# Optimization experiments

Measured on AMD Instinct MI355X. Metric: run time of the kernel, lower is better.

The kernel has to match this reference:

```python
import jax, jax.numpy as jnp
import numpy as np

# ---- static config (matches PFNet init) ----
B, N, F = 8, 5000, 15          # batch, num_max_elems, raw features
NUM_CLS_IN = 12                # elem_labels
NUM_CLS_OUT = 8                # class_labels
NUM_MOM = 3
H = 256                        # hidden_dim_id = hidden_dim_reg = distance_dim
BIN_SIZE = 500
N_BINS = N // BIN_SIZE         # 10
MAX_NUM_BINS = 200
K_NN = 16                      # num_neighbors
DIST_MULT = 0.1
ENC_DIM = NUM_CLS_IN + (F - 1)  # 26


def _dense_init(key, shape, scale=0.05):
    return scale * jax.random.normal(key, shape, dtype=jnp.float32)


def setup_inputs() -> dict:
    key = jax.random.key(0)
    ks = jax.random.split(key, 32)
    # X: col0 = integer element type id, rest = continuous features
    ids = jax.random.randint(ks[0], (B, N, 1), 0, NUM_CLS_IN).astype(jnp.float32)
    props = jax.random.normal(ks[1], (B, N, F - 1), dtype=jnp.float32)
    X = jnp.concatenate([ids, props], axis=-1)
    inp = {"X": X}
    # distance-embedding FFN (point_wise_feed_forward_network(distance_dim, dff))
    inp["ffn1_w"] = _dense_init(ks[2], (ENC_DIM, H)); inp["ffn1_b"] = jnp.zeros((H,), jnp.float32)
    inp["ffn2_w"] = _dense_init(ks[3], (H, H));       inp["ffn2_b"] = jnp.zeros((H,), jnp.float32)
    # LSH codebook rotations (non-trainable)
    inp["R"] = _dense_init(ks[4], (H, MAX_NUM_BINS // 2), scale=1.0)
    # id branch: encoder -> GHConv -> decoder -> logits
    inp["enc_id_w"] = _dense_init(ks[5], (ENC_DIM, H)); inp["enc_id_b"] = jnp.zeros((H,), jnp.float32)
    inp["wt_id"] = _dense_init(ks[6], (H, H)); inp["bt_id"] = _dense_init(ks[7], (H,))
    inp["wh_id"] = _dense_init(ks[8], (H, H)); inp["theta_id"] = _dense_init(ks[9], (H, H))
    inp["dec_id_w"] = _dense_init(ks[10], (H, H)); inp["dec_id_b"] = jnp.zeros((H,), jnp.float32)
    inp["out_id_w"] = _dense_init(ks[11], (H, NUM_CLS_OUT)); inp["out_id_b"] = jnp.zeros((NUM_CLS_OUT,), jnp.float32)
    # reg branch: takes concat(encoded, id_logits)
    inp["enc_reg_w"] = _dense_init(ks[12], (ENC_DIM + NUM_CLS_OUT, H)); inp["enc_reg_b"] = jnp.zeros((H,), jnp.float32)
    inp["wt_reg"] = _dense_init(ks[13], (H, H)); inp["bt_reg"] = _dense_init(ks[14], (H,))
    inp["wh_reg"] = _dense_init(ks[15], (H, H)); inp["theta_reg"] = _dense_init(ks[16], (H, H))
    inp["dec_reg_w"] = _dense_init(ks[17], (H, H)); inp["dec_reg_b"] = jnp.zeros((H,), jnp.float32)
    inp["out_reg_w"] = _dense_init(ks[18], (H, NUM_MOM)); inp["out_reg_b"] = jnp.zeros((NUM_MOM,), jnp.float32)
    return inp


def _build_knn_graph(points, R):
    """LSH-binned approximate kNN for one event. points: [N, H].
    Returns edge list (src, dst, vals), each [N_BINS*BIN_SIZE*K_NN]."""
    mul = points @ R[:, : N_BINS // 2]                 # [N, nbins/2]
    cmul = jnp.concatenate([mul, -mul], axis=-1)       # [N, nbins]
    bin_idx = jnp.argmax(cmul, axis=-1)
    bins_split = jnp.argsort(bin_idx).reshape(N_BINS, BIN_SIZE)   # [nb, bs]
    parts = points[bins_split]                         # [nb, bs, H]
    # pairwise distance inside each bin
    sq = jnp.sum(parts * parts, axis=-1)               # [nb, bs]
    d2 = sq[:, :, None] - 2.0 * jnp.einsum('bnd,bmd->bnm', parts, parts) + sq[:, None, :]
    dm = jnp.exp(-DIST_MULT * jnp.sqrt(jnp.maximum(d2, 1e-6)))    # [nb, bs, bs]
    vals, idx = jax.lax.top_k(dm, K_NN)                # [nb, bs, k] local indices
    dst = bins_split[jnp.arange(N_BINS)[:, None, None], idx]      # global dst
    src = jnp.broadcast_to(bins_split[:, :, None], idx.shape)     # global src
    return src.reshape(-1).astype(jnp.int32), dst.reshape(-1).astype(jnp.int32), vals.reshape(-1)


def _ghconv(x, src, dst, vals, W_t, b_t, W_h, theta):
    """GHConv for one event. x: [N, H]; edge list from _build_knn_graph.
    Duplicate edges sum, matching tf.sparse.add semantics."""
    deg = jax.ops.segment_sum(jnp.abs(vals), src, num_segments=N)          # row sums
    norm = jnp.power(deg + 1e-6, -0.5)[:, None]                            # [N, 1]
    f_hom = (x @ theta) * norm                                             # [N, H]
    msg = vals[:, None] * f_hom[dst]                                       # [E, H]
    f_hom = jax.ops.segment_sum(msg, src, num_segments=N) * norm
    f_het = x @ W_h
    gate = jax.nn.sigmoid(x @ W_t + b_t)
    return jax.nn.selu(gate * f_hom + (1.0 - gate) * f_het)


def reference(X, ffn1_w, ffn1_b, ffn2_w, ffn2_b, R,
              enc_id_w, enc_id_b, wt_id, bt_id, wh_id, theta_id,
              dec_id_w, dec_id_b, out_id_w, out_id_b,
              enc_reg_w, enc_reg_b, wt_reg, bt_reg, wh_reg, theta_reg,
              dec_reg_w, dec_reg_b, out_reg_w, out_reg_b):
    # InputEncoding: one-hot id + continuous props
    Xid = jax.nn.one_hot(jax.lax.stop_gradient(X[:, :, 0]).astype(jnp.int32), NUM_CLS_IN, dtype=jnp.float32)
    enc = jnp.concatenate([Xid, X[:, :, 1:]], axis=-1)                     # [B, N, 26]
    # distance embedding FFN (elu hidden)
    x_dist = jax.nn.elu(enc @ ffn1_w + ffn1_b) @ ffn2_w + ffn2_b           # [B, N, H]
    # LSH-binned approximate kNN graph per event
    src, dst, vals = jax.vmap(_build_knn_graph, in_axes=(0, None))(x_dist, R)
    # --- id branch ---
    h = jax.nn.selu(enc @ enc_id_w + enc_id_b)
    h = jax.vmap(_ghconv, in_axes=(0, 0, 0, 0, None, None, None, None))(
        h, src, dst, vals, wt_id, bt_id, wh_id, theta_id)
    h = jax.nn.selu(h @ dec_id_w + dec_id_b)
    out_id_logits = h @ out_id_w + out_id_b                                # [B, N, 8]
    xr = jnp.concatenate([enc, out_id_logits], axis=-1)                    # [B, N, 34]
    g = jax.nn.selu(xr @ enc_reg_w + enc_reg_b)
    g = jax.vmap(_ghconv, in_axes=(0, 0, 0, 0, None, None, None, None))(
        g, src, dst, vals, wt_reg, bt_reg, wh_reg, theta_reg)
    g = jax.nn.selu(g @ dec_reg_w + dec_reg_b)
    pred_momentum = g @ out_reg_w + out_reg_b                              # [B, N, 3]
    return out_id_logits, pred_momentum
```

## Files before the change

kernel.cpp:

```cpp
#include <hip/hip_runtime.h>
#include <math.h>

#define B_    8
#define N_    5000
#define F_    15
#define NCIN  12
#define NCOUT 8
#define NMOM  3
#define H_    256
#define BINSZ 500
#define NBINS 10
#define KNN   16
#define ENCD  26
#define XRD   34
#define M_TOT (B_*N_)

typedef unsigned short u16;
typedef _Float16 half8 __attribute__((ext_vector_type(8)));
typedef float f32x4_ __attribute__((ext_vector_type(4)));

__device__ __forceinline__ float elu_f(float x){ return x > 0.f ? x : expm1f(x); }
__device__ __forceinline__ float selu_f(float x){
    const float scale = 1.0507009873554804934193349852946f;
    const float alpha = 1.6732632423543772848170429916717f;
// ... 231 lines not shown
    const u16* Brow = Wt + (size_t)(n0 + mloc)*K;
    f32x4_ z = {0.f, 0.f, 0.f, 0.f};
    f32x4_ acc[4][4];
    #pragma unroll
    for (int i = 0; i < 4; ++i)
        #pragma unroll
        for (int j = 0; j < 4; ++j) acc[i][j] = z;
    const int fr = lane & 15, fks = lane >> 4;
    int nc = K >> 5;
    uint4 sa0, sa1, sb0, sb1;

    sa0 = *(const uint4*)(Arow + ksl*8);
    sa1 = *(const uint4*)(Arow + 16 + ksl*8);
    sb0 = *(const uint4*)(Brow + ksl*8);
    sb1 = *(const uint4*)(Brow + 16 + ksl*8);
    *(uint4*)ALS_(0,ksl,  mloc) = sa0;
    *(uint4*)ALS_(0,ksl+2,mloc) = sa1;
    *(uint4*)BLS_(0,ksl,  mloc) = sb0;
    *(uint4*)BLS_(0,ksl+2,mloc) = sb1;
    __syncthreads();

    for (int c = 0; c < nc; ++c){
        if (c + 1 < nc){
            int k0 = (c+1)*32;
            sa0 = *(const uint4*)(Arow + k0 + ksl*8);
            sa1 = *(const uint4*)(Arow + k0 + 16 + ksl*8);
            sb0 = *(const uint4*)(Brow + k0 + ksl*8);
            sb1 = *(const uint4*)(Brow + k0 + 16 + ksl*8);
        }
        int cb = c & 1;
        half8 af[4], bf[4];
        #pragma unroll
        for (int mi = 0; mi < 4; ++mi)
            af[mi] = *reinterpret_cast<const half8*>(ALS_(cb, fks, wr + mi*16 + fr));
        #pragma unroll
        for (int ni = 0; ni < 4; ++ni)
            bf[ni] = *reinterpret_cast<const half8*>(BLS_(cb, fks, wc + ni*16 + fr));
        #pragma unroll
        for (int mi = 0; mi < 4; ++mi)
            #pragma unroll
            for (int ni = 0; ni < 4; ++ni)
                acc[mi][ni] = __builtin_amdgcn_mfma_f32_16x16x32_f16(af[mi], bf[ni], acc[mi][ni], 0, 0, 0);
        if (c + 1 < nc){
            __syncthreads();
            int nb2 = (c+1) & 1;
            *(uint4*)ALS_(nb2,ksl,  mloc) = sa0;
            *(uint4*)ALS_(nb2,ksl+2,mloc) = sa1;
            *(uint4*)BLS_(nb2,ksl,  mloc) = sb0;
            *(uint4*)BLS_(nb2,ksl+2,mloc) = sb1;
            __syncthreads();
        }
    }
    if (Cb){
        __syncthreads();
        #pragma unroll
        for (int ni = 0; ni < 4; ++ni){
            int lc = wc + ni*16 + fr;
            float bv = bias ? bias[n0 + lc] : 0.f;
            #pragma unroll
            for (int mi = 0; mi < 4; ++mi)
                #pragma unroll
                for (int r = 0; r < 4; ++r){
                    int lrow = wr + mi*16 + fks*4 + r;
                    float v = acc[mi][ni][r] + bv;
                    if (ACT == 2) v = selu_f(v);
                    else if (ACT == 3) v = sigmoid_f(v);
                    smem[lrow*128 + lc] = f2h(v);
                }
        }
        __syncthreads();
        int colb = (lane & 15)*8;
        #pragma unroll
        for (int it = 0; it < 8; ++it){
            int lrow = w*32 + it*4 + (lane >> 4);
            int grow = m0 + lrow;
            if (grow < M)
                *(uint4*)&Cb[(size_t)grow*Nw + n0 + colb] = *(uint4*)&smem[lrow*128 + colb];
        }
    } else {
        #pragma unroll
        for (int ni = 0; ni < 4; ++ni){
            int col = n0 + wc + ni*16 + fr;
            float bv = bias ? bias[col] : 0.f;
            #pragma unroll
            for (int mi = 0; mi < 4; ++mi)
                #pragma unroll
                for (int r = 0; r < 4; ++r){
                    int row = m0 + wr + mi*16 + fks*4 + r;
                    if (row < M){
                        float v = acc[mi][ni][r] + bv;
                        if (ACT == 2) v = selu_f(v);
                        else if (ACT == 3) v = sigmoid_f(v);
                        Cf[(size_t)row*Nw + col] = v;
                    }
                }
        }
    }
    #undef ALS_
    #undef BLS_
}

__global__ __launch_bounds__(256) void k_gemm_f16x3(const u16* __restrict__ A,
        const u16* __restrict__ Wtcat, const float* __restrict__ bt,
        u16* __restrict__ G, u16* __restrict__ Hh, u16* __restrict__ Hm, int M){
    const int K = H_;
    __shared__ u16 smem[16384];
    #define ALS_(cb,ks,m) (smem +        ((cb)*4096 + (ks)*1024 + (m)*8))
    #define BLS_(cb,ks,m) (smem + 8192 + ((cb)*4096 + (ks)*1024 + (m)*8))
    int tid = threadIdx.x;
    int lane = tid & 63, w = tid >> 6;
    int wr = (w >> 1)*64, wc = (w & 1)*64;
    int lin = blockIdx.x;
    int xcd = lin & 7, jj = lin >> 3;
    int wk = (xcd < 6 ? xcd*235 : 6*235 + (xcd-6)*234) + jj;
    int m0 = (wk/6)*128;
    int yy = wk % 6;
    int seg = yy >> 1;
    u16* Cb = seg == 0 ? G : (seg == 1 ? Hh : Hm);
    int c0 = (yy & 1)*128;
    int n0 = yy*128;
    int mloc = tid & 127;
    int ksl  = tid >> 7;
    int gmA = m0 + mloc; if (gmA >= M) gmA = M - 1;
    const u16* Arow = A     + (size_t)gmA*K;
    const u16* Brow = Wtcat + (size_t)(n0 + mloc)*K;
    f32x4_ z = {0.f, 0.f, 0.f, 0.f};
    f32x4_ acc[4][4];
    #pragma unroll
    for (int i = 0; i < 4; ++i)
        #pragma unroll
        for (int j = 0; j < 4; ++j) acc[i][j] = z;
    const int fr = lane & 15, fks = lane >> 4;
    const int nc = K >> 5;
    uint4 sa0, sa1, sb0, sb1;
    sa0 = *(const uint4*)(Arow + ksl*8);
    sa1 = *(const uint4*)(Arow + 16 + ksl*8);
    sb0 = *(const uint4*)(Brow + ksl*8);
    sb1 = *(const uint4*)(Brow + 16 + ksl*8);
    *(uint4*)ALS_(0,ksl,  mloc) = sa0;
    *(uint4*)ALS_(0,ksl+2,mloc) = sa1;
    *(uint4*)BLS_(0,ksl,  mloc) = sb0;
    *(uint4*)BLS_(0,ksl+2,mloc) = sb1;
    __syncthreads();
    for (int c = 0; c < nc; ++c){
        if (c + 1 < nc){
            int k0 = (c+1)*32;
            sa0 = *(const uint4*)(Arow + k0 + ksl*8);
            sa1 = *(const uint4*)(Arow + k0 + 16 + ksl*8);
            sb0 = *(const uint4*)(Brow + k0 + ksl*8);
            sb1 = *(const uint4*)(Brow + k0 + 16 + ksl*8);
        }
        int cb = c & 1;
        half8 af[4], bf[4];
        #pragma unroll
        for (int mi = 0; mi < 4; ++mi)
            af[mi] = *reinterpret_cast<const half8*>(ALS_(cb, fks, wr + mi*16 + fr));
        #pragma unroll
        for (int ni = 0; ni < 4; ++ni)
            bf[ni] = *reinterpret_cast<const half8*>(BLS_(cb, fks, wc + ni*16 + fr));
        #pragma unroll
        for (int mi = 0; mi < 4; ++mi)
            #pragma unroll
            for (int ni = 0; ni < 4; ++ni)
                acc[mi][ni] = __builtin_amdgcn_mfma_f32_16x16x32_f16(af[mi], bf[ni], acc[mi][ni], 0, 0, 0);
        if (c + 1 < nc){
            __syncthreads();
            int nb2 = (c+1) & 1;
            *(uint4*)ALS_(nb2,ksl,  mloc) = sa0;
            *(uint4*)ALS_(nb2,ksl+2,mloc) = sa1;
            *(uint4*)BLS_(nb2,ksl,  mloc) = sb0;
            *(uint4*)BLS_(nb2,ksl+2,mloc) = sb1;
            __syncthreads();
        }
    }
    __syncthreads();
    #pragma unroll
    for (int ni = 0; ni < 4; ++ni){
        int lc = wc + ni*16 + fr;
        float bv = (seg == 0 && bt) ? bt[c0 + lc] : 0.f;
        #pragma unroll
        for (int mi = 0; mi < 4; ++mi)
            #pragma unroll
            for (int r = 0; r < 4; ++r){
                int lrow = wr + mi*16 + fks*4 + r;
                float v = acc[mi][ni][r] + bv;
                if (seg == 0) v = sigmoid_f(v);
                smem[lrow*128 + lc] = f2h(v);
            }
    }
    __syncthreads();
    int colb = (lane & 15)*8;
    #pragma unroll
    for (int it = 0; it < 8; ++it){
        int lrow = w*32 + it*4 + (lane >> 4);
        int grow = m0 + lrow;
        if (grow < M)
            *(uint4*)&Cb[(size_t)grow*H_ + c0 + colb] = *(uint4*)&smem[lrow*128 + colb];
    }
    #undef ALS_
    #undef BLS_
}

__global__ void k_gemm_small(const u16* __restrict__ A, const float* __restrict__ W,
        const float* __restrict__ bias, float* __restrict__ C, int M, int K, int Nw){
    int t = blockIdx.x*blockDim.x + threadIdx.x;
    if (t >= M*Nw) return;
    int m = t / Nw, c = t % Nw;
    const u16* a = A + (size_t)m*K;
    float acc = 0.f;
    for (int k = 0; k < K; k += 8){
        uint4 u = *(const uint4*)(a + k);
        const u16* us = (const u16*)&u;
        #pragma unroll
        for (int j = 0; j < 8; ++j) acc += h2f(us[j]) * W[(k+j)*Nw + c];
    }
    C[t] = acc + bias[c];
}

__global__ __launch_bounds__(256) void k_bins(const float* __restrict__ xd,
        const float* __restrict__ Rt, int* __restrict__ bin_idx){
    int g = blockIdx.x*4 + (threadIdx.x >> 6);
    int lane = threadIdx.x & 63;
    const float4* p = (const float4*)(xd + (size_t)g*H_);
    float4 x = p[lane];
    float acc[5];
    #pragma unroll
    for (int j = 0; j < 5; ++j){
        float4 r = ((const float4*)(Rt + j*H_))[lane];
        acc[j] = x.x*r.x + x.y*r.y + x.z*r.z + x.w*r.w;
    }
    #pragma unroll
    for (int off = 32; off; off >>= 1)
        #pragma unroll
        for (int j = 0; j < 5; ++j) acc[j] += __shfl_xor(acc[j], off, 64);
    if (lane == 0){
        float best = acc[0]; int bi = 0;
        #pragma unroll
        for (int j = 1; j < 5; ++j) if (acc[j] > best){ best = acc[j]; bi = j; }
        #pragma unroll
        for (int j = 0; j < 5; ++j){ float v = -acc[j]; if (v > best){ best = v; bi = 5 + j; } }
        bin_idx[g] = bi;
    }
}

__global__ __launch_bounds__(256) void k_sort(const int* __restrict__ bin_idx,
                                              int* __restrict__ order){
    int b = blockIdx.x;
    const int* bi = bin_idx + b*N_;
    int* ord = order + b*N_;
    __shared__ int cnt[256][NBINS];
    __shared__ int binoff[NBINS];
    int t = threadIdx.x;
    const int CH = (N_ + 255)/256;
    int lo = t*CH, hi = lo+CH < N_ ? lo+CH : N_;
    for (int j = 0; j < NBINS; ++j) cnt[t][j] = 0;
    for (int n = lo; n < hi; ++n) cnt[t][bi[n]]++;
    __syncthreads();
    if (t < NBINS){
        int run = 0;
        for (int q = 0; q < 256; ++q){ int v = cnt[q][t]; cnt[q][t] = run; run += v; }
        binoff[t] = run;
    }
    __syncthreads();
    if (t == 0){
        int run = 0;
        for (int j = 0; j < NBINS; ++j){ int v = binoff[j]; binoff[j] = run; run += v; }
    }
    __syncthreads();
    for (int n = lo; n < hi; ++n){
        int v = bi[n];
        int pos = binoff[v] + cnt[t][v]++;
        ord[pos] = n;
    }
}

__global__ __launch_bounds__(256) void k_gather(const float* __restrict__ xd,
        const int* __restrict__ order, u16* __restrict__ xh, u16* __restrict__ xl,
        float* __restrict__ sqg){
    int g = blockIdx.x*4 + (threadIdx.x >> 6);
    int lane = threadIdx.x & 63;
    int b = g / N_;
    int node = order[g];
    const float4* src = (const float4*)(xd + ((size_t)b*N_ + node)*H_);
    float4 v = src[lane];
    unsigned hw0, hw1, lw0, lw1;
    {
        u16 h0 = f2h(v.x), h1 = f2h(v.y), h2 = f2h(v.z), h3 = f2h(v.w);
        u16 l0 = f2h(v.x - h2f(h0)), l1 = f2h(v.y - h2f(h1));
        u16 l2 = f2h(v.z - h2f(h2)), l3 = f2h(v.w - h2f(h3));
        hw0 = (unsigned)h0 | ((unsigned)h1 << 16);
        hw1 = (unsigned)h2 | ((unsigned)h3 << 16);
        lw0 = (unsigned)l0 | ((unsigned)l1 << 16);
        lw1 = (unsigned)l2 | ((unsigned)l3 << 16);
    }
    uint2 hw = {hw0, hw1}, lw = {lw0, lw1};
    *(uint2*)(xh + (size_t)g*H_ + lane*4) = hw;
    *(uint2*)(xl + (size_t)g*H_ + lane*4) = lw;
    float s = v.x*v.x + v.y*v.y + v.z*v.z + v.w*v.w;
    #pragma unroll
    for (int off = 32; off; off >>= 1) s += __shfl_xor(s, off, 64);
    if (lane == 0) sqg[g] = s;
}

__global__ __launch_bounds__(256) void k_dist(const u16* __restrict__ xh,
        const u16* __restrict__ xl, const float* __restrict__ sqg,
        float* __restrict__ dm){
    int lin = blockIdx.x;
    int wk = (lin & 7)*160 + (lin >> 3);
    int binlin = wk >> 4;
    int tile = wk & 15;
    int tr = (tile >> 2)*128, tc = (tile & 3)*128;
    const u16* xhb = xh + (size_t)binlin*BINSZ*H_;
    const u16* xlb = xl + (size_t)binlin*BINSZ*H_;
    const float* sqb = sqg + binlin*BINSZ;
    __shared__ u16 Ah[4][128][8], Al[4][128][8];
    __shared__ u16 Bh[4][128][8], Bl[4][128][8];
    __shared__ float sqr[128], sqc[128];
    int tid = threadIdx.x;
    if (tid < 128){ int r = tr + tid; sqr[tid] = sqb[r < BINSZ ? r : BINSZ-1]; }
    else { int c = tc + (tid-128); sqc[tid-128] = sqb[c < BINSZ ? c : BINSZ-1]; }
    int lane = tid & 63, w = tid >> 6;
    int wr = (w >> 1)*64, wc = (w & 1)*64;
    int mloc = tid & 127, ksl = tid >> 7;
    int rA = tr + mloc; if (rA >= BINSZ) rA = BINSZ-1;
    int rC = tc + mloc; if (rC >= BINSZ) rC = BINSZ-1;
    const u16* ArH = xhb + (size_t)rA*H_ + ksl*8;
    const u16* ArL = xlb + (size_t)rA*H_ + ksl*8;
    const u16* BrH = xhb + (size_t)rC*H_ + ksl*8;
    const u16* BrL = xlb + (size_t)rC*H_ + ksl*8;
    f32x4_ z = {0.f, 0.f, 0.f, 0.f};
    f32x4_ acc[4][4];
    #pragma unroll
    for (int i = 0; i < 4; ++i)
        #pragma unroll
        for (int j = 0; j < 4; ++j) acc[i][j] = z;
    const int fr = lane & 15, fks = lane >> 4;
    uint4 pah0, pah1, pal0, pal1, pbh0, pbh1, pbl0, pbl1;

    pah0 = *(const uint4*)(ArH);      pah1 = *(const uint4*)(ArH + 16);
    pal0 = *(const uint4*)(ArL);      pal1 = *(const uint4*)(ArL + 16);
    pbh0 = *(const uint4*)(BrH);      pbh1 = *(const uint4*)(BrH + 16);
    pbl0 = *(const uint4*)(BrL);      pbl1 = *(const uint4*)(BrL + 16);
    *(uint4*)(&Ah[ksl  ][mloc][0]) = pah0;
    *(uint4*)(&Ah[ksl+2][mloc][0]) = pah1;
    *(uint4*)(&Al[ksl  ][mloc][0]) = pal0;
    *(uint4*)(&Al[ksl+2][mloc][0]) = pal1;
    *(uint4*)(&Bh[ksl  ][mloc][0]) = pbh0;
    *(uint4*)(&Bh[ksl+2][mloc][0]) = pbh1;
    *(uint4*)(&Bl[ksl  ][mloc][0]) = pbl0;
    *(uint4*)(&Bl[ksl+2][mloc][0]) = pbl1;
    __syncthreads();

    const int NCH = H_/32;
    for (int cc = 0; cc < NCH; ++cc){
        if (cc + 1 < NCH){
            int k0 = (cc+1)*32;
            pah0 = *(const uint4*)(ArH + k0);      pah1 = *(const uint4*)(ArH + k0 + 16);
            pal0 = *(const uint4*)(ArL + k0);      pal1 = *(const uint4*)(ArL + k0 + 16);
            pbh0 = *(const uint4*)(BrH + k0);      pbh1 = *(const uint4*)(BrH + k0 + 16);
            pbl0 = *(const uint4*)(BrL + k0);      pbl1 = *(const uint4*)(BrL + k0 + 16);
        }
        half8 afh[4], afl[4];
        #pragma unroll
        for (int mi = 0; mi < 4; ++mi){
            afh[mi] = *reinterpret_cast<const half8*>(&Ah[fks][wr + mi*16 + fr][0]);
            afl[mi] = *reinterpret_cast<const half8*>(&Al[fks][wr + mi*16 + fr][0]);
        }
        #pragma unroll
        for (int ni = 0; ni < 4; ++ni){
            half8 bfh = *reinterpret_cast<const half8*>(&Bh[fks][wc + ni*16 + fr][0]);
            half8 bfl = *reinterpret_cast<const half8*>(&Bl[fks][wc + ni*16 + fr][0]);
            #pragma unroll
            for (int mi = 0; mi < 4; ++mi){
                acc[mi][ni] = __builtin_amdgcn_mfma_f32_16x16x32_f16(afh[mi], bfh, acc[mi][ni], 0, 0, 0);
                acc[mi][ni] = __builtin_amdgcn_mfma_f32_16x16x32_f16(afh[mi], bfl, acc[mi][ni], 0, 0, 0);
                acc[mi][ni] = __builtin_amdgcn_mfma_f32_16x16x32_f16(afl[mi], bfh, acc[mi][ni], 0, 0, 0);
            }
        }
        if (cc + 1 < NCH){
            __syncthreads();
            *(uint4*)(&Ah[ksl  ][mloc][0]) = pah0;
            *(uint4*)(&Ah[ksl+2][mloc][0]) = pah1;
            *(uint4*)(&Al[ksl  ][mloc][0]) = pal0;
            *(uint4*)(&Al[ksl+2][mloc][0]) = pal1;
            *(uint4*)(&Bh[ksl  ][mloc][0]) = pbh0;
            *(uint4*)(&Bh[ksl+2][mloc][0]) = pbh1;
            *(uint4*)(&Bl[ksl  ][mloc][0]) = pbl0;
            *(uint4*)(&Bl[ksl+2][mloc][0]) = pbl1;
            __syncthreads();
        }
    }
    #pragma unroll
    for (int mi = 0; mi < 4; ++mi){
        #pragma unroll
        for (int r = 0; r < 4; ++r){
            int lr = wr + mi*16 + fks*4 + r;
            int rg = tr + lr;
            if (rg >= BINSZ) continue;
            float sr = sqr[lr];
            #pragma unroll
            for (int ni = 0; ni < 4; ++ni){
                int lc = wc + ni*16 + fr;
                int c = tc + lc;
                if (c >= BINSZ) continue;
                float d2 = sr - 2.f*acc[mi][ni][r] + sqc[lc];
                dm[((size_t)binlin*BINSZ + rg)*BINSZ + c] = d2;
            }
        }
    }
}

__global__ __launch_bounds__(256) void k_sel(const float* __restrict__ dmraw,
        const int* __restrict__ order,
        int* __restrict__ nbr_idx, float* __restrict__ nbr_val,
        float* __restrict__ nrm){
    int wid = blockIdx.x*4 + (threadIdx.x >> 6);
    int lane = threadIdx.x & 63;
    int half = lane >> 5;
    int l32  = lane & 31;
    int g = wid*2 + half;
    int b = g / N_, pos = g % N_;
    int bin = pos / BINSZ, r = pos % BINSZ;
    int binlin = b*NBINS + bin;
    const float* row = dmraw + ((size_t)binlin*BINSZ + r)*BINSZ;

    typedef unsigned long long u64;
    #define LOADK(i) u64 k##i; { int c = l32 + (i)*32; \
        if (c < BINSZ){ unsigned db = __float_as_uint(fmaxf(row[c], 1e-6f)); \
            k##i = ((u64)db << 32) | (unsigned)c; } else k##i = ~0ull; }
    LOADK(0) LOADK(1) LOADK(2)  LOADK(3)  LOADK(4)  LOADK(5)  LOADK(6)  LOADK(7)
    LOADK(8) LOADK(9) LOADK(10) LOADK(11) LOADK(12) LOADK(13) LOADK(14) LOADK(15)
    #undef LOADK

    #define CSU(a,b) { u64 mn_ = a < b ? a : b; u64 mx_ = a < b ? b : a; a = mn_; b = mx_; }
    #define CSD(a,b) { u64 mn_ = a < b ? a : b; u64 mx_ = a < b ? b : a; a = mx_; b = mn_; }
    CSU(k0,k1) CSD(k2,k3) CSU(k4,k5) CSD(k6,k7) CSU(k8,k9) CSD(k10,k11) CSU(k12,k13) CSD(k14,k15)
    CSU(k0,k2) CSU(k1,k3) CSD(k4,k6) CSD(k5,k7) CSU(k8,k10) CSU(k9,k11) CSD(k12,k14) CSD(k13,k15)
    CSU(k0,k1) CSU(k2,k3) CSD(k4,k5) CSD(k6,k7) CSU(k8,k9) CSU(k10,k11) CSD(k12,k13) CSD(k14,k15)
    CSU(k0,k4) CSU(k1,k5) CSU(k2,k6) CSU(k3,k7) CSD(k8,k12) CSD(k9,k13) CSD(k10,k14) CSD(k11,k15)
    CSU(k0,k2) CSU(k1,k3) CSU(k4,k6) CSU(k5,k7) CSD(k8,k10) CSD(k9,k11) CSD(k12,k14) CSD(k13,k15)
    CSU(k0,k1) CSU(k2,k3) CSU(k4,k5) CSU(k6,k7) CSD(k8,k9) CSD(k10,k11) CSD(k12,k13) CSD(k14,k15)
    CSU(k0,k8) CSU(k1,k9) CSU(k2,k10) CSU(k3,k11) CSU(k4,k12) CSU(k5,k13) CSU(k6,k14) CSU(k7,k15)
    CSU(k0,k4) CSU(k1,k5) CSU(k2,k6)  CSU(k3,k7)  CSU(k8,k12) CSU(k9,k13) CSU(k10,k14) CSU(k11,k15)
    CSU(k0,k2) CSU(k1,k3) CSU(k4,k6)  CSU(k5,k7)  CSU(k8,k10) CSU(k9,k11) CSU(k12,k14) CSU(k13,k15)
    CSU(k0,k1) CSU(k2,k3) CSU(k4,k5)  CSU(k6,k7)  CSU(k8,k9)  CSU(k10,k11) CSU(k12,k13) CSU(k14,k15)
    #undef CSU
    #undef CSD

    u64 mykey = ~0ull;
    #pragma unroll
    for (int rr = 0; rr < KNN; ++rr){
        u64 m = k0;
        #pragma unroll
        for (int off = 16; off; off >>= 1){
            u64 o = __shfl_xor(m, off, 64);
            if (o < m) m = o;
        }
        if (l32 == rr) mykey = m;
        bool win = (k0 == m);
        k0  = win ? k1  : k0;
        k1  = win ? k2  : k1;
        k2  = win ? k3  : k2;
        k3  = win ? k4  : k3;
        k4  = win ? k5  : k4;
        k5  = win ? k6  : k5;
        k6  = win ? k7  : k6;
        k7  = win ? k8  : k7;
        k8  = win ? k9  : k8;
        k9  = win ? k10 : k9;
        k10 = win ? k11 : k10;
        k11 = win ? k12 : k11;
        k12 = win ? k13 : k12;
        k13 = win ? k14 : k13;
        k14 = win ? k15 : k14;
        k15 = win ? ~0ull : k15;
    }
    float myd = __uint_as_float((unsigned)(mykey >> 32));
    int myc = (int)(unsigned)(mykey & 0xFFFFFFFFull);
    float myv = (l32 < KNN) ? expf(-0.1f*sqrtf(myd)) : 0.f;
    float deg = myv;
    #pragma unroll
    for (int off = 16; off; off >>= 1) deg += __shfl_xor(deg, off, 64);
    const int* ord = order + b*N_ + bin*BINSZ;
    int node_i = ord[r];
    if (l32 < KNN){
        nbr_idx[((size_t)b*N_ + node_i)*KNN + l32] = ord[myc];
        nbr_val[((size_t)b*N_ + node_i)*KNN + l32] = myv;
    }
    if (l32 == 0) nrm[b*N_ + node_i] = 1.f/sqrtf(deg + 1e-6f);
}

__global__ __launch_bounds__(256) void k_ghconv(const u16* __restrict__ gate,
        const u16* __restrict__ het, const u16* __restrict__ hom,
        const int* __restrict__ nbr_idx, const float* __restrict__ nbr_val,
        const float* __restrict__ nrm, u16* __restrict__ out){
    int node = blockIdx.x;
    int b = node / N_;
    int t = threadIdx.x;
    __shared__ int nid[KNN];
    __shared__ float nv[KNN];
    if (t < KNN){
        int d = nbr_idx[(size_t)node*KNN + t];
        nid[t] = d;
        nv[t] = nbr_val[(size_t)node*KNN + t] * nrm[b*N_ + d];
    }
    __syncthreads();
    float acc = 0.f;
    #pragma unroll
    for (int k = 0; k < KNN; ++k)
        acc += nv[k] * h2f(hom[((size_t)b*N_ + nid[k])*H_ + t]);
    float ni = nrm[node];
    float g = h2f(gate[(size_t)node*H_ + t]);
    float v = g * (ni * acc) + (1.f - g) * h2f(het[(size_t)node*H_ + t]);
    out[(size_t)node*H_ + t] = f2h(selu_f(v));
}

__global__ void k_xr(const float* __restrict__ enc, const float* __restrict__ logits,
                     u16* __restrict__ xr_h){
    int i = blockIdx.x*blockDim.x + threadIdx.x;
    if (i >= M_TOT) return;
    const float* e = enc + (size_t)i*ENCD;
    const float* l = logits + (size_t)i*NCOUT;
    u16* x = xr_h + (size_t)i*64;
    #pragma unroll
    for (int j = 0; j < ENCD; ++j) x[j] = f2h(e[j]);
    #pragma unroll
    for (int j = 0; j < NCOUT; ++j) x[ENCD+j] = f2h(l[j]);
    #pragma unroll
    for (int j = XRD; j < 64; ++j) x[j] = 0;
}

extern "C" void kernel_launch(void* const* d_in, const int* in_sizes, int n_in,
                              void* d_out, int out_size, void* d_ws, size_t ws_size,
                              hipStream_t stream){
    const float* X        = (const float*)d_in[0];
    const float* ffn1_w   = (const float*)d_in[1];
    const float* ffn1_b   = (const float*)d_in[2];
    const float* ffn2_w   = (const float*)d_in[3];
    const float* ffn2_b   = (const float*)d_in[4];
    const float* R        = (const float*)d_in[5];
    const float* enc_id_w = (const float*)d_in[6];
    const float* enc_id_b = (const float*)d_in[7];
    const float* wt_id    = (const float*)d_in[8];
    const float* bt_id    = (const float*)d_in[9];
    const float* wh_id    = (const float*)d_in[10];
    const float* theta_id = (const float*)d_in[11];
    const float* dec_id_w = (const float*)d_in[12];
    const float* dec_id_b = (const float*)d_in[13];
    const float* out_id_w = (const float*)d_in[14];
    const float* out_id_b = (const float*)d_in[15];
    const float* enc_reg_w= (const float*)d_in[16];
    const float* enc_reg_b= (const float*)d_in[17];
    const float* wt_reg   = (const float*)d_in[18];
    const float* bt_reg   = (const float*)d_in[19];
    const float* wh_reg   = (const float*)d_in[20];
    const float* theta_reg= (const float*)d_in[21];
    const float* dec_reg_w= (const float*)d_in[22];
    const float* dec_reg_b= (const float*)d_in[23];
    const float* out_reg_w= (const float*)d_in[24];
    const float* out_reg_b= (const float*)d_in[25];

    float* out_logits = (float*)d_out;
    float* out_mom    = (float*)d_out + (size_t)M_TOT*NCOUT;

    float* ws = (float*)d_ws;
    size_t o = 0;
    float* enc  = ws + o; o += (size_t)M_TOT*ENCD;
    float* bufC = ws + o; o += (size_t)M_TOT*H_;
    float* bufB = ws + o; o += (size_t)M_TOT*H_;
    float* bufD = ws + o; o += (size_t)M_TOT*H_;
    float* sqg  = ws + o; o += M_TOT;
    float* nrm  = ws + o; o += M_TOT;
    float* nbrv = ws + o; o += (size_t)M_TOT*KNN;
    float* Rt   = ws + o; o += 5*H_;
    int* ibase   = (int*)(ws + o);
    o += (size_t)18*M_TOT;
    int* bin_idx = ibase;
    int* order   = ibase + M_TOT;
    int* nbr_idx = ibase + 2*M_TOT;
    u16* hbase = (u16*)(ws + o);
    size_t ho = 0;
    u16* enc_h = hbase + ho; ho += (size_t)M_TOT*32;
    u16* enc_l = hbase + ho; ho += (size_t)M_TOT*32;
    u16* xr_h  = hbase + ho; ho += (size_t)M_TOT*64;
    u16* hA_h  = hbase + ho; ho += (size_t)M_TOT*H_;
    u16* h1_h  = hbase + ho; ho += (size_t)M_TOT*H_;
    u16* wt_encid  = hbase + ho; ho += 256*32;
    u16* wt_encreg = hbase + ho; ho += 256*64;
    u16* wtcat_id  = hbase + ho; ho += (size_t)768*256;
    u16* dec_id_h  = hbase + ho; ho += (size_t)256*256;
    u16* wtcat_reg = hbase + ho; ho += (size_t)768*256;
    u16* dec_reg_h = hbase + ho; ho += (size_t)256*256;
    u16* wf1h = hbase + ho; ho += 256*32;
    u16* wf1l = hbase + ho; ho += 256*32;
    u16* wf2h = hbase + ho; ho += (size_t)256*256;
    u16* wf2l = hbase + ho; ho += (size_t)256*256;
    u16* h1h = (u16*)bufC;
    u16* h1l = h1h + (size_t)M_TOT*H_;
    u16* xh = (u16*)bufC;
    u16* xl = xh + (size_t)M_TOT*H_;
    float* dm = bufB;
    u16* gate_h = (u16*)bufC;
    u16* het_h  = gate_h + (size_t)M_TOT*H_;
    u16* hom_h  = (u16*)bufB;

    PrepArgs pa;
    const float* srcs[NPREP] = {enc_id_w, enc_reg_w, wt_id, wh_id, theta_id, dec_id_w,
                                wt_reg, wh_reg, theta_reg, dec_reg_w,
                                ffn1_w, ffn1_w, ffn2_w, ffn2_w};
    u16* dsts[NPREP] = {wt_encid, wt_encreg, wtcat_id, wtcat_id + 65536, wtcat_id + 131072,
                        dec_id_h, wtcat_reg, wtcat_reg + 65536, wtcat_reg + 131072, dec_reg_h,
                        wf1h, wf1l, wf2h, wf2l};
    int Ks[NPREP]  = {ENCD, XRD, H_, H_, H_, H_, H_, H_, H_, H_, ENCD, ENCD, H_, H_};
    int Kas[NPREP] = {32, 64, H_, H_, H_, H_, H_, H_, H_, H_, 32, 32, H_, H_};
    int los[NPREP] = {0,0,0,0,0,0,0,0,0,0, 0,1,0,1};
    int acc_blk = 0;
    for (int i = 0; i < NPREP; ++i){
        pa.src[i] = srcs[i]; pa.dst[i] = dsts[i]; pa.K[i] = Ks[i]; pa.Ka[i] = Kas[i];
        pa.lo[i] = los[i];
        acc_blk += Kas[i];
        pa.blk_end[i] = acc_blk;
    }

    dim3 b256(256);
    int nb = (M_TOT + 255)/256;
    dim3 gf(M_TOT/64, H_/128);

    k_prep<<<acc_blk, b256, 0, stream>>>(pa);
    k_prepR<<<5, b256, 0, stream>>>(R, Rt);
    k_encode<<<nb, b256, 0, stream>>>(X, enc, enc_h, enc_l);

    k_ffn<1,1><<<gf, b256, 0, stream>>>(enc_h, enc_l, wf1h, wf1l, ffn1_b,
                                        nullptr, h1h, h1l, M_TOT, 32, H_);
    k_ffn<0,0><<<gf, b256, 0, stream>>>(h1h, h1l, wf2h, wf2l, ffn2_b,
                                        bufB, nullptr, nullptr, M_TOT, H_, H_);

    k_bins<<<M_TOT/4, b256, 0, stream>>>(bufB, Rt, bin_idx);
    k_sort<<<B_, b256, 0, stream>>>(bin_idx, order);
    k_gather<<<M_TOT/4, b256, 0, stream>>>(bufB, order, xh, xl, sqg);
    k_dist<<<1280, b256, 0, stream>>>(xh, xl, sqg, dm);
    k_sel<<<M_TOT/8, b256, 0, stream>>>(dm, order, nbr_idx, nbrv, nrm);

    k_gemm_f16<2><<<626, b256, 0, stream>>>(enc_h, wt_encid, enc_id_b, nullptr, hA_h, M_TOT, 32, H_);
    k_gemm_f16x3<<<1878, b256, 0, stream>>>(hA_h, wtcat_id, bt_id, gate_h, het_h, hom_h, M_TOT);
    k_ghconv<<<M_TOT, b256, 0, stream>>>(gate_h, het_h, hom_h, nbr_idx, nbrv, nrm, h1_h);
    k_gemm_f16<2><<<626, b256, 0, stream>>>(h1_h, dec_id_h, dec_id_b, nullptr, hA_h, M_TOT, H_, H_);
    k_gemm_small<<<(M_TOT*NCOUT + 255)/256, b256, 0, stream>>>(hA_h, out_id_w, out_id_b,
                                                               out_logits, M_TOT, H_, NCOUT);

    k_xr<<<nb, b256, 0, stream>>>(enc, out_logits, xr_h);
    k_gemm_f16<2><<<626, b256, 0, stream>>>(xr_h, wt_encreg, enc_reg_b, nullptr, h1_h, M_TOT, 64, H_);
    k_gemm_f16x3<<<1878, b256, 0, stream>>>(h1_h, wtcat_reg, bt_reg, gate_h, het_h, hom_h, M_TOT);
    k_ghconv<<<M_TOT, b256, 0, stream>>>(gate_h, het_h, hom_h, nbr_idx, nbrv, nrm, hA_h);
    k_gemm_f16<2><<<626, b256, 0, stream>>>(hA_h, dec_reg_h, dec_reg_b, nullptr, h1_h, M_TOT, H_, H_);
    k_gemm_small<<<(M_TOT*NMOM + 255)/256, b256, 0, stream>>>(h1_h, out_reg_w, out_reg_b,
                                                              out_mom, M_TOT, H_, NMOM);

    (void)in_sizes; (void)n_in; (void)out_size; (void)ws_size;
}
```

Before: 493.6 us.

## Fuse pairwise distance computation with top-k neighbor selection via shared memory

Merges the binned distance-matrix kernel and the kNN selection kernel into one. Each block computes a 16-row strip of squared distances against all 500 bin columns with MFMA, keeps the strip in shared memory, then runs the bitonic top-16 selection on it. This removes the round trip of the full distance matrix through global memory. In exchange, the column operands are reloaded for every 16-row strip, each block does less MFMA work, and shared memory use per block is larger.

```diff
diff --git a/kernel.cpp b/kernel.cpp
--- a/kernel.cpp
+++ b/kernel.cpp
@@ -557,192 +557,155 @@
     if (lane == 0) sqg[g] = s;
 }
 
-__global__ __launch_bounds__(256) void k_dist(const u16* __restrict__ xh,
+__global__ __launch_bounds__(256) void k_distsel(const u16* __restrict__ xh,
         const u16* __restrict__ xl, const float* __restrict__ sqg,
-        float* __restrict__ dm){
+        const int* __restrict__ order,
+        int* __restrict__ nbr_idx, float* __restrict__ nbr_val,
+        float* __restrict__ nrm){
     int lin = blockIdx.x;
-    int wk = (lin & 7)*160 + (lin >> 3);
-    int binlin = wk >> 4;
-    int tile = wk & 15;
-    int tr = (tile >> 2)*128, tc = (tile & 3)*128;
+    int wk = (lin & 7)*320 + (lin >> 3);
+    int binlin = wk >> 5;
+    int rg = wk & 31;
+    int tr = rg*16;
+    int b = binlin / NBINS, bin = binlin % NBINS;
     const u16* xhb = xh + (size_t)binlin*BINSZ*H_;
     const u16* xlb = xl + (size_t)binlin*BINSZ*H_;
     const float* sqb = sqg + binlin*BINSZ;
-    __shared__ u16 Ah[4][128][8], Al[4][128][8];
-    __shared__ u16 Bh[4][128][8], Bl[4][128][8];
-    __shared__ float sqr[128], sqc[128];
+
+    __shared__ float d2buf[16][516];
+    __shared__ u16 Ch_[4][128][8], Cl_[4][128][8];
+    __shared__ u16 Rh_[4][16][8],  Rl_[4][16][8];
+    __shared__ float sqc_s[512];
+    __shared__ float sqr_s[16];
+
     int tid = threadIdx.x;
-    if (tid < 128){ int r = tr + tid; sqr[tid] = sqb[r < BINSZ ? r : BINSZ-1]; }
-    else { int c = tc + (tid-128); sqc[tid-128] = sqb[c < BINSZ ? c : BINSZ-1]; }
     int lane = tid & 63, w = tid >> 6;
-    int wr = (w >> 1)*64, wc = (w & 1)*64;
-    int mloc = tid & 127, ksl = tid >> 7;
-    int rA = tr + mloc; if (rA >= BINSZ) rA = BINSZ-1;
-    int rC = tc + mloc; if (rC >= BINSZ) rC = BINSZ-1;
-    const u16* ArH = xhb + (size_t)rA*H_ + ksl*8;
-    const u16* ArL = xlb + (size_t)rA*H_ + ksl*8;
-    const u16* BrH = xhb + (size_t)rC*H_ + ksl*8;
-    const u16* BrL = xlb + (size_t)rC*H_ + ksl*8;
-    f32x4_ z = {0.f, 0.f, 0.f, 0.f};
-    f32x4_ acc[4][4];
-    #pragma unroll
-    for (int i = 0; i < 4; ++i)
-        #pragma unroll
-        for (int j = 0; j < 4; ++j) acc[i][j] = z;
     const int fr = lane & 15, fks = lane >> 4;
-    uint4 pah0, pah1, pal0, pal1, pbh0, pbh1, pbl0, pbl1;
-
-    pah0 = *(const uint4*)(ArH);      pah1 = *(const uint4*)(ArH + 16);
-    pal0 = *(const uint4*)(ArL);      pal1 = *(const uint4*)(ArL + 16);
-    pbh0 = *(const uint4*)(BrH);      pbh1 = *(const uint4*)(BrH + 16);
-    pbl0 = *(const uint4*)(BrL);      pbl1 = *(const uint4*)(BrL + 16);
-    *(uint4*)(&Ah[ksl  ][mloc][0]) = pah0;
-    *(uint4*)(&Ah[ksl+2][mloc][0]) = pah1;
-    *(uint4*)(&Al[ksl  ][mloc][0]) = pal0;
-    *(uint4*)(&Al[ksl+2][mloc][0]) = pal1;
-    *(uint4*)(&Bh[ksl  ][mloc][0]) = pbh0;
-    *(uint4*)(&Bh[ksl+2][mloc][0]) = pbh1;
-    *(uint4*)(&Bl[ksl  ][mloc][0]) = pbl0;
-    *(uint4*)(&Bl[ksl+2][mloc][0]) = pbl1;
-    __syncthreads();
-
-    const int NCH = H_/32;
-    for (int cc = 0; cc < NCH; ++cc){
-        if (cc + 1 < NCH){
-            int k0 = (cc+1)*32;
-            pah0 = *(const uint4*)(ArH + k0);      pah1 = *(const uint4*)(ArH + k0 + 16);
-            pal0 = *(const uint4*)(ArL + k0);      pal1 = *(const uint4*)(ArL + k0 + 16);
-            pbh0 = *(const uint4*)(BrH + k0);      pbh1 = *(const uint4*)(BrH + k0 + 16);
-            pbl0 = *(const uint4*)(BrL + k0);      pbl1 = *(const uint4*)(BrL + k0 + 16);
-        }
-        half8 afh[4], afl[4];
-        #pragma unroll
-        for (int mi = 0; mi < 4; ++mi){
-            afh[mi] = *reinterpret_cast<const half8*>(&Ah[fks][wr + mi*16 + fr][0]);
-            afl[mi] = *reinterpret_cast<const half8*>(&Al[fks][wr + mi*16 + fr][0]);
-        }
-        #pragma unroll
-        for (int ni = 0; ni < 4; ++ni){
-            half8 bfh = *reinterpret_cast<const half8*>(&Bh[fks][wc + ni*16 + fr][0]);
-            half8 bfl = *reinterpret_cast<const half8*>(&Bl[fks][wc + ni*16 + fr][0]);
-            #pragma unroll
-            for (int mi = 0; mi < 4; ++mi){
-                acc[mi][ni] = __builtin_amdgcn_mfma_f32_16x16x32_f16(afh[mi], bfh, acc[mi][ni], 0, 0, 0);
-                acc[mi][ni] = __builtin_amdgcn_mfma_f32_16x16x32_f16(afh[mi], bfl, acc[mi][ni], 0, 0, 0);
-                acc[mi][ni] = __builtin_amdgcn_mfma_f32_16x16x32_f16(afl[mi], bfh, acc[mi][ni], 0, 0, 0);
+
+    for (int c = tid; c < BINSZ; c += 256) sqc_s[c] = sqb[c];
+    if (tid < 16){ int r = tr + tid; sqr_s[tid] = sqb[r < BINSZ ? r : BINSZ-1]; }
+
+    int s0 = w*2, s1 = w*2 + 1;
+
+    for (int ct = 0; ct < 4; ++ct){
+        int c0 = ct*128;
+        f32x4_ acc0 = {0.f,0.f,0.f,0.f}, acc1 = {0.f,0.f,0.f,0.f};
+        for (int kc = 0; kc < 8; ++kc){
+            __syncthreads();
+            #pragma unroll
+            for (int i = 0; i < 2; ++i){
+                int idx = tid + i*256;
+                int col = idx >> 2, ks = idx & 3;
+                int gc = c0 + col; if (gc >= BINSZ) gc = BINSZ-1;
+                *(uint4*)(&Ch_[ks][col][0]) = *(const uint4*)(xhb + (size_t)gc*H_ + kc*32 + ks*8);
+                *(uint4*)(&Cl_[ks][col][0]) = *(const uint4*)(xlb + (size_t)gc*H_ + kc*32 + ks*8);
             }
-        }
-        if (cc + 1 < NCH){
+            if (tid < 64){
+                int row = tid >> 2, ks = tid & 3;
+                int gr = tr + row; if (gr >= BINSZ) gr = BINSZ-1;
+                *(uint4*)(&Rh_[ks][row][0]) = *(const uint4*)(xhb + (size_t)gr*H_ + kc*32 + ks*8);
+                *(uint4*)(&Rl_[ks][row][0]) = *(const uint4*)(xlb + (size_t)gr*H_ + kc*32 + ks*8);
+            }
             __syncthreads();
-            *(uint4*)(&Ah[ksl  ][mloc][0]) = pah0;
-            *(uint4*)(&Ah[ksl+2][mloc][0]) = pah1;
-            *(uint4*)(&Al[ksl  ][mloc][0]) = pal0;
-            *(uint4*)(&Al[ksl+2][mloc][0]) = pal1;
-            *(uint4*)(&Bh[ksl  ][mloc][0]) = pbh0;
-            *(uint4*)(&Bh[ksl+2][mloc][0]) = pbh1;
-            *(uint4*)(&Bl[ksl  ][mloc][0]) = pbl0;
-            *(uint4*)(&Bl[ksl+2][mloc][0]) = pbl1;
-            __syncthreads();
-        }
-    }
-    #pragma unroll
-    for (int mi = 0; mi < 4; ++mi){
+            half8 rh = *reinterpret_cast<const half8*>(&Rh_[fks][fr][0]);
+            half8 rl = *reinterpret_cast<const half8*>(&Rl_[fks][fr][0]);
+            half8 c0h = *reinterpret_cast<const half8*>(&Ch_[fks][s0*16 + fr][0]);
+            half8 c0l = *reinterpret_cast<const half8*>(&Cl_[fks][s0*16 + fr][0]);
+            half8 c1h = *reinterpret_cast<const half8*>(&Ch_[fks][s1*16 + fr][0]);
+            half8 c1l = *reinterpret_cast<const half8*>(&Cl_[fks][s1*16 + fr][0]);
+            acc0 = __builtin_amdgcn_mfma_f32_16x16x32_f16(rh, c0h, acc0, 0, 0, 0);
+            acc0 = __builtin_amdgcn_mfma_f32_16x16x32_f16(rh, c0l, acc0, 0, 0, 0);
+            acc0 = __builtin_amdgcn_mfma_f32_16x16x32_f16(rl, c0h, acc0, 0, 0, 0);
+            acc1 = __builtin_amdgcn_mfma_f32_16x16x32_f16(rh, c1h, acc1, 0, 0, 0);
+            acc1 = __builtin_amdgcn_mfma_f32_16x16x32_f16(rh, c1l, acc1, 0, 0, 0);
+            acc1 = __builtin_amdgcn_mfma_f32_16x16x32_f16(rl, c1h, acc1, 0, 0, 0);
+        }
         #pragma unroll
         for (int r = 0; r < 4; ++r){
-            int lr = wr + mi*16 + fks*4 + r;
-            int rg = tr + lr;
-            if (rg >= BINSZ) continue;
-            float sr = sqr[lr];
-            #pragma unroll
-            for (int ni = 0; ni < 4; ++ni){
-                int lc = wc + ni*16 + fr;
-                int c = tc + lc;
-                if (c >= BINSZ) continue;
-                float d2 = sr - 2.f*acc[mi][ni][r] + sqc[lc];
-                dm[((size_t)binlin*BINSZ + rg)*BINSZ + c] = d2;
+            int row = fks*4 + r;
+            float sr = sqr_s[row];
+            int lc0 = c0 + s0*16 + fr;
+            if (lc0 < BINSZ) d2buf[row][s0*16 + fr + c0] = sr - 2.f*acc0[r] + sqc_s[lc0];
+            int lc1 = c0 + s1*16 + fr;
+            if (lc1 < BINSZ) d2buf[row][s1*16 + fr + c0] = sr - 2.f*acc1[r] + sqc_s[lc1];
+        }
+    }
+    __syncthreads();
+
+    typedef unsigned long long u64;
+    const int* ord = order + b*N_ + bin*BINSZ;
+    #pragma unroll
+    for (int p = 0; p < 2; ++p){
+        int lrow = p*8 + w*2 + (lane >> 5);
+        int l32  = lane & 31;
+        int pos  = tr + lrow;
+        const float* row = &d2buf[lrow][0];
+
+        #define LOADK(i) u64 k##i; { int c = l32 + (i)*32; \
+            if (c < BINSZ){ unsigned db = __float_as_uint(fmaxf(row[c], 1e-6f)); \
+                k##i = ((u64)db << 32) | (unsigned)c; } else k##i = ~0ull; }
+        LOADK(0) LOADK(1) LOADK(2)  LOADK(3)  LOADK(4)  LOADK(5)  LOADK(6)  LOADK(7)
+        LOADK(8) LOADK(9) LOADK(10) LOADK(11) LOADK(12) LOADK(13) LOADK(14) LOADK(15)
+        #undef LOADK
+
+        #define CSU(a,b) { u64 mn_ = a < b ? a : b; u64 mx_ = a < b ? b : a; a = mn_; b = mx_; }
+        #define CSD(a,b) { u64 mn_ = a < b ? a : b; u64 mx_ = a < b ? b : a; a = mx_; b = mn_; }
+        CSU(k0,k1) CSD(k2,k3) CSU(k4,k5) CSD(k6,k7) CSU(k8,k9) CSD(k10,k11) CSU(k12,k13) CSD(k14,k15)
+        CSU(k0,k2) CSU(k1,k3) CSD(k4,k6) CSD(k5,k7) CSU(k8,k10) CSU(k9,k11) CSD(k12,k14) CSD(k13,k15)
+        CSU(k0,k1) CSU(k2,k3) CSD(k4,k5) CSD(k6,k7) CSU(k8,k9) CSU(k10,k11) CSD(k12,k13) CSD(k14,k15)
+        CSU(k0,k4) CSU(k1,k5) CSU(k2,k6) CSU(k3,k7) CSD(k8,k12) CSD(k9,k13) CSD(k10,k14) CSD(k11,k15)
+        CSU(k0,k2) CSU(k1,k3) CSU(k4,k6) CSU(k5,k7) CSD(k8,k10) CSD(k9,k11) CSD(k12,k14) CSD(k13,k15)
+        CSU(k0,k1) CSU(k2,k3) CSU(k4,k5) CSU(k6,k7) CSD(k8,k9) CSD(k10,k11) CSD(k12,k13) CSD(k14,k15)
+        CSU(k0,k8) CSU(k1,k9) CSU(k2,k10) CSU(k3,k11) CSU(k4,k12) CSU(k5,k13) CSU(k6,k14) CSU(k7,k15)
+        CSU(k0,k4) CSU(k1,k5) CSU(k2,k6)  CSU(k3,k7)  CSU(k8,k12) CSU(k9,k13) CSU(k10,k14) CSU(k11,k15)
+        CSU(k0,k2) CSU(k1,k3) CSU(k4,k6)  CSU(k5,k7)  CSU(k8,k10) CSU(k9,k11) CSU(k12,k14) CSU(k13,k15)
+        CSU(k0,k1) CSU(k2,k3) CSU(k4,k5)  CSU(k6,k7)  CSU(k8,k9)  CSU(k10,k11) CSU(k12,k13) CSU(k14,k15)
+        #undef CSU
+        #undef CSD
+
+        u64 mykey = ~0ull;
+        #pragma unroll
+        for (int rr = 0; rr < KNN; ++rr){
+            u64 m = k0;
+            #pragma unroll
+            for (int off = 16; off; off >>= 1){
+                u64 o = __shfl_xor(m, off, 64);
+                if (o < m) m = o;
             }
-        }
-    }
-}
-
-__global__ __launch_bounds__(256) void k_sel(const float* __restrict__ dmraw,
-        const int* __restrict__ order,
-        int* __restrict__ nbr_idx, float* __restrict__ nbr_val,
-        float* __restrict__ nrm){
-    int wid = blockIdx.x*4 + (threadIdx.x >> 6);
-    int lane = threadIdx.x & 63;
-    int half = lane >> 5;
-    int l32  = lane & 31;
-    int g = wid*2 + half;
-    int b = g / N_, pos = g % N_;
-    int bin = pos / BINSZ, r = pos % BINSZ;
-    int binlin = b*NBINS + bin;
-    const float* row = dmraw + ((size_t)binlin*BINSZ + r)*BINSZ;
-
-    typedef unsigned long long u64;
-    #define LOADK(i) u64 k##i; { int c = l32 + (i)*32; \
-        if (c < BINSZ){ unsigned db = __float_as_uint(fmaxf(row[c], 1e-6f)); \
-            k##i = ((u64)db << 32) | (unsigned)c; } else k##i = ~0ull; }
-    LOADK(0) LOADK(1) LOADK(2)  LOADK(3)  LOADK(4)  LOADK(5)  LOADK(6)  LOADK(7)
-    LOADK(8) LOADK(9) LOADK(10) LOADK(11) LOADK(12) LOADK(13) LOADK(14) LOADK(15)
-    #undef LOADK
-
-    #define CSU(a,b) { u64 mn_ = a < b ? a : b; u64 mx_ = a < b ? b : a; a = mn_; b = mx_; }
-    #define CSD(a,b) { u64 mn_ = a < b ? a : b; u64 mx_ = a < b ? b : a; a = mx_; b = mn_; }
-    CSU(k0,k1) CSD(k2,k3) CSU(k4,k5) CSD(k6,k7) CSU(k8,k9) CSD(k10,k11) CSU(k12,k13) CSD(k14,k15)
-    CSU(k0,k2) CSU(k1,k3) CSD(k4,k6) CSD(k5,k7) CSU(k8,k10) CSU(k9,k11) CSD(k12,k14) CSD(k13,k15)
-    CSU(k0,k1) CSU(k2,k3) CSD(k4,k5) CSD(k6,k7) CSU(k8,k9) CSU(k10,k11) CSD(k12,k13) CSD(k14,k15)
-    CSU(k0,k4) CSU(k1,k5) CSU(k2,k6) CSU(k3,k7) CSD(k8,k12) CSD(k9,k13) CSD(k10,k14) CSD(k11,k15)
-    CSU(k0,k2) CSU(k1,k3) CSU(k4,k6) CSU(k5,k7) CSD(k8,k10) CSD(k9,k11) CSD(k12,k14) CSD(k13,k15)
-    CSU(k0,k1) CSU(k2,k3) CSU(k4,k5) CSU(k6,k7) CSD(k8,k9) CSD(k10,k11) CSD(k12,k13) CSD(k14,k15)
-    CSU(k0,k8) CSU(k1,k9) CSU(k2,k10) CSU(k3,k11) CSU(k4,k12) CSU(k5,k13) CSU(k6,k14) CSU(k7,k15)
-    CSU(k0,k4) CSU(k1,k5) CSU(k2,k6)  CSU(k3,k7)  CSU(k8,k12) CSU(k9,k13) CSU(k10,k14) CSU(k11,k15)
-    CSU(k0,k2) CSU(k1,k3) CSU(k4,k6)  CSU(k5,k7)  CSU(k8,k10) CSU(k9,k11) CSU(k12,k14) CSU(k13,k15)
-    CSU(k0,k1) CSU(k2,k3) CSU(k4,k5)  CSU(k6,k7)  CSU(k8,k9)  CSU(k10,k11) CSU(k12,k13) CSU(k14,k15)
-    #undef CSU
-    #undef CSD
-
-    u64 mykey = ~0ull;
-    #pragma unroll
-    for (int rr = 0; rr < KNN; ++rr){
-        u64 m = k0;
-        #pragma unroll
-        for (int off = 16; off; off >>= 1){
-            u64 o = __shfl_xor(m, off, 64);
-            if (o < m) m = o;
-        }
-        if (l32 == rr) mykey = m;
-        bool win = (k0 == m);
-        k0  = win ? k1  : k0;
-        k1  = win ? k2  : k1;
-        k2  = win ? k3  : k2;
-        k3  = win ? k4  : k3;
-        k4  = win ? k5  : k4;
-        k5  = win ? k6  : k5;
-        k6  = win ? k7  : k6;
-        k7  = win ? k8  : k7;
-        k8  = win ? k9  : k8;
-        k9  = win ? k10 : k9;
-        k10 = win ? k11 : k10;
-        k11 = win ? k12 : k11;
-        k12 = win ? k13 : k12;
-        k13 = win ? k14 : k13;
-        k14 = win ? k15 : k14;
-        k15 = win ? ~0ull : k15;
-    }
-    float myd = __uint_as_float((unsigned)(mykey >> 32));
-    int myc = (int)(unsigned)(mykey & 0xFFFFFFFFull);
-    float myv = (l32 < KNN) ? expf(-0.1f*sqrtf(myd)) : 0.f;
-    float deg = myv;
-    #pragma unroll
-    for (int off = 16; off; off >>= 1) deg += __shfl_xor(deg, off, 64);
-    const int* ord = order + b*N_ + bin*BINSZ;
-    int node_i = ord[r];
-    if (l32 < KNN){
-        nbr_idx[((size_t)b*N_ + node_i)*KNN + l32] = ord[myc];
-        nbr_val[((size_t)b*N_ + node_i)*KNN + l32] = myv;
-    }
-    if (l32 == 0) nrm[b*N_ + node_i] = 1.f/sqrtf(deg + 1e-6f);
+            if (l32 == rr) mykey = m;
+            bool win = (k0 == m);
+            k0  = win ? k1  : k0;
+            k1  = win ? k2  : k1;
+            k2  = win ? k3  : k2;
+            k3  = win ? k4  : k3;
+            k4  = win ? k5  : k4;
+            k5  = win ? k6  : k5;
+            k6  = win ? k7  : k6;
+            k7  = win ? k8  : k7;
+            k8  = win ? k9  : k8;
+            k9  = win ? k10 : k9;
+            k10 = win ? k11 : k10;
+            k11 = win ? k12 : k11;
+            k12 = win ? k13 : k12;
+            k13 = win ? k14 : k13;
+            k14 = win ? k15 : k14;
+            k15 = win ? ~0ull : k15;
+        }
+        float myd = __uint_as_float((unsigned)(mykey >> 32));
+        int myc = (int)(unsigned)(mykey & 0xFFFFFFFFull);
+        float myv = (l32 < KNN) ? expf(-0.1f*sqrtf(myd)) : 0.f;
+        float deg = myv;
+        #pragma unroll
+        for (int off = 16; off; off >>= 1) deg += __shfl_xor(deg, off, 64);
+        if (pos < BINSZ){
+            int node_i = ord[pos];
+            if (l32 < KNN){
+                nbr_idx[((size_t)b*N_ + node_i)*KNN + l32] = ord[myc];
+                nbr_val[((size_t)b*N_ + node_i)*KNN + l32] = myv;
+            }
+            if (l32 == 0) nrm[b*N_ + node_i] = 1.f/sqrtf(deg + 1e-6f);
+        }
+    }
 }
 
 __global__ __launch_bounds__(256) void k_ghconv(const u16* __restrict__ gate,
@@ -854,7 +817,6 @@
     u16* h1l = h1h + (size_t)M_TOT*H_;
     u16* xh = (u16*)bufC;
     u16* xl = xh + (size_t)M_TOT*H_;
-    float* dm = bufB;
     u16* gate_h = (u16*)bufC;
     u16* het_h  = gate_h + (size_t)M_TOT*H_;
     u16* hom_h  = (u16*)bufB;
@@ -893,8 +855,7 @@
     k_bins<<<M_TOT/4, b256, 0, stream>>>(bufB, Rt, bin_idx);
     k_sort<<<B_, b256, 0, stream>>>(bin_idx, order);
     k_gather<<<M_TOT/4, b256, 0, stream>>>(bufB, order, xh, xl, sqg);
-    k_dist<<<1280, b256, 0, stream>>>(xh, xl, sqg, dm);
-    k_sel<<<M_TOT/8, b256, 0, stream>>>(dm, order, nbr_idx, nbrv, nrm);
+    k_distsel<<<2560, b256, 0, stream>>>(xh, xl, sqg, order, nbr_idx, nbrv, nrm);
 
     k_gemm_f16<2><<<626, b256, 0, stream>>>(enc_h, wt_encid, enc_id_b, nullptr, hA_h, M_TOT, 32, H_);
     k_gemm_f16x3<<<1878, b256, 0, stream>>>(hA_h, wtcat_id, bt_id, gate_h, het_h, hom_h, M_TOT);
```

After: 561.2 us. +13.7%, slower.
